# Performance work log

Hardware: AMD Instinct MI355X
Metric: run time of the kernel (lower is better)

Reference implementation:

```python
import jax, jax.numpy as jnp
import numpy as np

EPS_PROJ = 0.004   # float32 branch of _project
EPS_MIN = 1e-15


def _poincare_linear(x, weight_v, weight_g, bias, c):
    c = c.reshape(())
    rc = jnp.sqrt(c)
    # z_unit: column-normalized weight (weight_v / ||weight_v||_col)
    z_unit = weight_v / jnp.maximum(jnp.linalg.norm(weight_v, axis=0), EPS_MIN)  # [in, out]
    # unidirectional Poincare MLR
    drcr = 2.0 * rc * bias                                  # [out]
    rcx = rc * x                                            # [N, in]
    cx2 = jnp.sum(rcx * rcx, axis=-1, keepdims=True)        # [N, 1]
    num = 2.0 * (rcx @ z_unit) * jnp.cosh(drcr) - (1.0 + cx2) * jnp.sinh(drcr)
    mlr = 2.0 * weight_g / rc * jnp.arcsinh(num / jnp.maximum(1.0 - cx2, EPS_MIN))  # [N, out]
    # map back to the ball: sinh, then gyro-half map
    y = jnp.sinh(rc * mlr) / rc
    y = y / (1.0 + jnp.sqrt(1.0 + c * jnp.sum(y * y, axis=-1, keepdims=True)))
    # _project onto ball of curvature k = -c
    k = -c
    maxnorm = (1.0 - EPS_PROJ) / jnp.sqrt(jnp.maximum(jnp.abs(k), EPS_MIN))
    maxnorm = jnp.where(k < 0, maxnorm, jnp.float32(1e15))
    norm = jnp.maximum(jnp.linalg.norm(y, axis=-1, keepdims=True), EPS_MIN)
    return jnp.where(norm > maxnorm, y / norm * maxnorm, y)


def setup_inputs() -> dict:
    key = jax.random.key(0)
    k1, k2, k3 = jax.random.split(key, 3)
    N, IN, OUT = 32768, 1024, 1024
    # points strictly inside the unit Poincare ball (||x|| ~ 0.64)
    x = jax.random.normal(k1, (N, IN), dtype=jnp.float32) * 0.02
    std = (2.0 * IN * OUT) ** (-0.5)
    weight_v = jax.random.normal(k2, (IN, OUT), dtype=jnp.float32) * std
    weight_g = jax.random.uniform(k3, (OUT,), dtype=jnp.float32, minval=0.5, maxval=1.5) * std * (IN ** 0.5)
    bias = jnp.zeros((OUT,), dtype=jnp.float32)
    c = jnp.ones((1,), dtype=jnp.float32)
    return {"x": x, "weight_v": weight_v, "weight_g": weight_g, "bias": bias, "c": c}


def reference(x, weight_v, weight_g, bias, c):
    return _poincare_linear(x, weight_v, weight_g, bias, c)
```

## Files before the change

kernel.cpp:

```cpp
#include <hip/hip_runtime.h>

#define K_DIM 1024
#define N_DIM 1024
#define GRID 256

typedef short v8s __attribute__((ext_vector_type(8)));
typedef float v4f __attribute__((ext_vector_type(4)));

__device__ __forceinline__ unsigned int bf16_rne(float f) {
    unsigned int u = __float_as_uint(f);
    u += 0x7FFFu + ((u >> 16) & 1u);
    return u >> 16;
}

__global__ void prep_w(const float* __restrict__ wv, const float* __restrict__ wg,
                       const float* __restrict__ bias, const float* __restrict__ cptr,
                       float* __restrict__ coshd, float* __restrict__ sinhd,
                       float* __restrict__ gfac, unsigned short* __restrict__ Btf) {
    __shared__ float tile[64 * 65];
    __shared__ float cred[4][64];
    __shared__ float cinv[64];
    const int t = threadIdx.x;
    const int ti = blockIdx.x & 15;
    const int tj = blockIdx.x >> 4;
    {
        const int cj = t & 63, rg = t >> 6;
        const float* wp = wv + (size_t)(rg * 256) * N_DIM + tj * 64 + cj;
        float ss = 0.f;
#pragma unroll 4
        for (int r = 0; r < 256; ++r) {
            float v = wp[(size_t)r * N_DIM];
            ss = fmaf(v, v, ss);
        }
        cred[rg][cj] = ss;
    }
    {
        const int kl = t >> 2, cq = t & 3;
        const float* src = wv + (size_t)(ti * 64 + kl) * N_DIM + tj * 64 + cq * 16;
        float4 fq[4];
#pragma unroll
        for (int i = 0; i < 4; ++i) fq[i] = ((const float4*)src)[i];
        float* dst = &tile[kl * 65 + cq * 16];
#pragma unroll
        for (int i = 0; i < 4; ++i) {
            dst[4 * i + 0] = fq[i].x; dst[4 * i + 1] = fq[i].y;
            dst[4 * i + 2] = fq[i].z; dst[4 * i + 3] = fq[i].w;
        }
    }
    __syncthreads();
    if (t < 64) {
        float s = cred[0][t] + cred[1][t] + cred[2][t] + cred[3][t];
        cinv[t] = 1.0f / fmaxf(sqrtf(s), 1e-15f);
        if (ti == 0) {
            const int col = tj * 64 + t;
            const float rc = sqrtf(cptr[0]);
            float d = 2.0f * rc * bias[col];
            float e = __expf(d), ie = 1.0f / e;
            coshd[col] = 0.5f * (e + ie);
            sinhd[col] = 0.5f * (e - ie);
            gfac[col] = 2.0f * wg[col];
        }
    }
    __syncthreads();
    {
        const int nl = t & 63, kc = t >> 6;
        const float ci = cinv[nl];
        const int nt_g = tj * 4 + (nl >> 4);
#pragma unroll
        for (int h = 0; h < 2; ++h) {
            const int k8g = ti * 8 + kc * 2 + h;
            const int ks_g = k8g >> 2;
            const int L = (nl & 15) | ((k8g & 3) << 4);
            unsigned int p[4];
#pragma unroll
            for (int j = 0; j < 4; ++j) {
                float v0 = tile[(kc * 16 + h * 8 + 2 * j) * 65 + nl] * ci;
                float v1 = tile[(kc * 16 + h * 8 + 2 * j + 1) * 65 + nl] * ci;
                p[j] = bf16_rne(v0) | (bf16_rne(v1) << 16);
            }
            *(uint4*)(Btf + ((size_t)(nt_g * 32 + ks_g) * 64 + L) * 8) =
                make_uint4(p[0], p[1], p[2], p[3]);
        }
    }
}

__device__ __forceinline__ void stage_panel(const float* __restrict__ xp,
                                            unsigned short* __restrict__ Asl,
                                            float* __restrict__ rowssbuf, int t) {
#pragma unroll 2
    for (int it = 0; it < 16; ++it) {
        const int g = it * 512 + t;
        const int row = g >> 7, k8 = g & 127;
        const float4* fp = (const float4*)xp + (size_t)g * 2;
        float4 f0 = fp[0];
        float4 f1 = fp[1];
        float vals[8] = {f0.x, f0.y, f0.z, f0.w, f1.x, f1.y, f1.z, f1.w};
        unsigned int p[4];
        float ss = 0.f;
#pragma unroll
        for (int j = 0; j < 4; ++j) {
            ss = fmaf(vals[2 * j], vals[2 * j], ss);
            ss = fmaf(vals[2 * j + 1], vals[2 * j + 1], ss);
            p[j] = bf16_rne(vals[2 * j]) | (bf16_rne(vals[2 * j + 1]) << 16);
        }
        ss += __shfl_xor(ss, 1);  ss += __shfl_xor(ss, 2);  ss += __shfl_xor(ss, 4);
        ss += __shfl_xor(ss, 8);  ss += __shfl_xor(ss, 16); ss += __shfl_xor(ss, 32);
        if ((t & 63) == 0) atomicAdd(&rowssbuf[row], ss);
        const int mt = row >> 4, lm2 = row & 15, ks = k8 >> 2, qq = k8 & 3;
        const int idx = ((mt * 32 + ks) * 512) + (((lm2 ^ (ks & 7)) | (qq << 4)) * 8);
        *(uint4*)&Asl[idx] = make_uint4(p[0], p[1], p[2], p[3]);
    }
}

__launch_bounds__(512, 2)
__global__ void gemm_fused(const float* __restrict__ x,
                           const unsigned short* __restrict__ Btf,
                           const float* __restrict__ cptr,
                           const float* __restrict__ coshd, const float* __restrict__ sinhd,
                           const float* __restrict__ gfac,
                           float* __restrict__ out, int panels) {
    __shared__ __align__(16) unsigned short As[4 * 32 * 512];
    __shared__ float s_rowss[2][64];
    __shared__ float s_rsum[64];

    const int t = threadIdx.x;
    const int w = t >> 6, L = t & 63;
    const int lm = L & 15, q = L >> 4;
    const int bm = blockIdx.x;

    const float cc = cptr[0];
    const float rc = sqrtf(cc);
    const float two_rc = 2.0f * rc;
    const float halfinvrc = 0.5f / rc;
    const float mn = (cc > 0.f) ? 0.996f / sqrtf(fmaxf(cc, 1e-15f)) : 1e15f;
    float ch[8], sh[8], gf[8];
#pragma unroll
    for (int n = 0; n < 8; ++n) {
        const int col = w * 128 + n * 16 + lm;
        ch[n] = coshd[col]; sh[n] = sinhd[col]; gf[n] = gfac[col];
    }

    const unsigned short* bw = Btf + (size_t)(w * 8) * 32 * 512 + (size_t)L * 8;

    if (t < 64) s_rowss[0][t] = 0.f;
    __syncthreads();
    stage_panel(x + (size_t)bm * 64 * K_DIM, As, s_rowss[0], t);

#pragma unroll 1
    for (int i = 0; i < panels; ++i) {
        const int p = bm + i * GRID;
        const int pb = i & 1, nb = pb ^ 1;
        const bool more = (i + 1 < panels);
        __syncthreads();

        v4f acc[4][8];
#pragma unroll
        for (int a = 0; a < 4; ++a)
#pragma unroll
            for (int b = 0; b < 8; ++b) acc[a][b] = (v4f){0.f, 0.f, 0.f, 0.f};

        v8s bA[8], bB[8];
#pragma unroll
        for (int n = 0; n < 8; ++n)
            bA[n] = *(const v8s*)(bw + (n * 32) * 512);

#pragma unroll 1
        for (int kp = 0; kp < 16; ++kp) {
            const int k0 = kp * 2;
#pragma unroll
            for (int n = 0; n < 8; ++n)
                bB[n] = *(const v8s*)(bw + (n * 32 + k0 + 1) * 512);
            {
                const int lx = ((lm ^ (k0 & 7)) | (q << 4)) * 8;
                v8s a[4];
#pragma unroll
                for (int mt = 0; mt < 4; ++mt)
                    a[mt] = *(const v8s*)&As[(mt * 32 + k0) * 512 + lx];
                __builtin_amdgcn_s_setprio(1);
#pragma unroll
                for (int mt = 0; mt < 4; ++mt)
#pragma unroll
                    for (int n = 0; n < 8; ++n)
                        acc[mt][n] = __builtin_amdgcn_mfma_f32_16x16x32_bf16(
                            a[mt], bA[n], acc[mt][n], 0, 0, 0);
                __builtin_amdgcn_s_setprio(0);
            }
            if (kp < 15) {
#pragma unroll
                for (int n = 0; n < 8; ++n)
                    bA[n] = *(const v8s*)(bw + (n * 32 + k0 + 2) * 512);
            }
            {
                const int lx = ((lm ^ ((k0 + 1) & 7)) | (q << 4)) * 8;
                v8s a[4];
#pragma unroll
                for (int mt = 0; mt < 4; ++mt)
                    a[mt] = *(const v8s*)&As[(mt * 32 + k0 + 1) * 512 + lx];
                __builtin_amdgcn_s_setprio(1);
#pragma unroll
                for (int mt = 0; mt < 4; ++mt)
#pragma unroll
                    for (int n = 0; n < 8; ++n)
                        acc[mt][n] = __builtin_amdgcn_mfma_f32_16x16x32_bf16(
                            a[mt], bB[n], acc[mt][n], 0, 0, 0);
                __builtin_amdgcn_s_setprio(0);
            }
        }

        __syncthreads();
        if (t < 64) { s_rsum[t] = 0.f; if (more) s_rowss[nb][t] = 0.f; }
        __syncthreads();

        if (more) stage_panel(x + (size_t)(p + GRID) * 64 * K_DIM, As, s_rowss[nb], t);

        const float* rb = s_rowss[pb];
#pragma unroll
        for (int mt = 0; mt < 4; ++mt) {
            const int mloc = mt * 16 + q * 4;
            float sx[4];
#pragma unroll
            for (int rr = 0; rr < 4; ++rr) sx[rr] = cc * rb[mloc + rr];
            float rs[4] = {0.f, 0.f, 0.f, 0.f};
#pragma unroll
            for (int n = 0; n < 8; ++n) {
                v4f d = acc[mt][n];
#pragma unroll
                for (int rr = 0; rr < 4; ++rr) {
                    float cx2 = sx[rr];
                    float num = two_rc * d[rr] * ch[n] - (1.0f + cx2) * sh[n];
                    float den = fmaxf(1.0f - cx2, 1e-15f);
                    float tt = num * __builtin_amdgcn_rcpf(den);
                    float as_ = __logf(fabsf(tt) + sqrtf(fmaf(tt, tt, 1.0f)));
                    as_ = copysignf(as_, tt);
                    float u = gf[n] * as_;
                    float e = __expf(u);
                    float y = (e - __builtin_amdgcn_rcpf(e)) * halfinvrc;
                    d[rr] = y;
                    rs[rr] = fmaf(y, y, rs[rr]);
                }
                acc[mt][n] = d;
            }
#pragma unroll
            for (int rr = 0; rr < 4; ++rr) {
                float v = rs[rr];
                v += __shfl_xor(v, 1); v += __shfl_xor(v, 2);
                v += __shfl_xor(v, 4); v += __shfl_xor(v, 8);
                if (lm == 0) atomicAdd(&s_rsum[mloc + rr], v);
            }
        }
        __syncthreads();

#pragma unroll
        for (int mt = 0; mt < 4; ++mt) {
            const int mloc = mt * 16 + q * 4;
            float f[4];
#pragma unroll
            for (int rr = 0; rr < 4; ++rr) {
                const float s = s_rsum[mloc + rr];
                const float scale = 1.0f / (1.0f + sqrtf(fmaf(cc, s, 1.0f)));
                const float nrm = fmaxf(sqrtf(s) * scale, 1e-15f);
                f[rr] = scale * (nrm > mn ? mn / nrm : 1.0f);
            }
#pragma unroll
            for (int rr = 0; rr < 4; ++rr) {
                float* op = out + (size_t)(p * 64 + mloc + rr) * N_DIM + w * 128 + lm;
#pragma unroll
                for (int n = 0; n < 8; ++n) op[n * 16] = acc[mt][n][rr] * f[rr];
            }
        }
    }
}

extern "C" void kernel_launch(void* const* d_in, const int* in_sizes, int n_in,
                              void* d_out, int out_size, void* d_ws, size_t ws_size,
                              hipStream_t stream) {
    const float* x    = (const float*)d_in[0];
    const float* wv   = (const float*)d_in[1];
    const float* wg   = (const float*)d_in[2];
    const float* bias = (const float*)d_in[3];
    const float* cptr = (const float*)d_in[4];
    float* out = (float*)d_out;

    const int OUT = in_sizes[2];
    const int IN  = in_sizes[1] / OUT;
    const int M   = in_sizes[0] / IN;

    float* coshd = (float*)d_ws;
    float* sinhd = coshd + 1024;
    float* gfac  = sinhd + 1024;
    unsigned short* Btf = (unsigned short*)(gfac + 1024);

    prep_w<<<(IN / 64) * (OUT / 64), 256, 0, stream>>>(
        wv, wg, bias, cptr, coshd, sinhd, gfac, Btf);

    const int panels = (M / 64) / GRID;
    gemm_fused<<<GRID, 512, 0, stream>>>(
        x, Btf, cptr, coshd, sinhd, gfac, out, panels);
}
```

Before: 371.0 us.

## Hand-pipeline B global loads with inline asm and explicit vmcnt waits, new LDS swizzle

Rewrites the GEMM inner loop as an explicit two-stage software pipeline. B fragments are loaded with inline global_load_dwordx4 from a scalar base plus per-lane offsets, and waits use explicit s_waitcnt vmcnt(8) with sched barriers so one k-step of loads stays in flight during the MFMAs. The A panel LDS layout gets a new XOR swizzle that also uses the quad index, to cut LDS bank conflicts, and the staging loop unroll goes from 2 to 4. Hand-written waitcnt and asm constrain the compiler's scheduling and depend on exact counts of in-flight loads.

```diff
diff --git a/kernel.cpp b/kernel.cpp
--- a/kernel.cpp
+++ b/kernel.cpp
@@ -6,6 +6,7 @@
 
 typedef short v8s __attribute__((ext_vector_type(8)));
 typedef float v4f __attribute__((ext_vector_type(4)));
+typedef unsigned int v4u __attribute__((ext_vector_type(4)));
 
 __device__ __forceinline__ unsigned int bf16_rne(float f) {
     unsigned int u = __float_as_uint(f);
@@ -87,7 +88,7 @@
 __device__ __forceinline__ void stage_panel(const float* __restrict__ xp,
                                             unsigned short* __restrict__ Asl,
                                             float* __restrict__ rowssbuf, int t) {
-#pragma unroll 2
+#pragma unroll 4
     for (int it = 0; it < 16; ++it) {
         const int g = it * 512 + t;
         const int row = g >> 7, k8 = g & 127;
@@ -106,11 +107,44 @@
         ss += __shfl_xor(ss, 1);  ss += __shfl_xor(ss, 2);  ss += __shfl_xor(ss, 4);
         ss += __shfl_xor(ss, 8);  ss += __shfl_xor(ss, 16); ss += __shfl_xor(ss, 32);
         if ((t & 63) == 0) atomicAdd(&rowssbuf[row], ss);
-        const int mt = row >> 4, lm2 = row & 15, ks = k8 >> 2, qq = k8 & 3;
-        const int idx = ((mt * 32 + ks) * 512) + (((lm2 ^ (ks & 7)) | (qq << 4)) * 8);
+        const int mt = row >> 4, lmr = row & 15, ks = k8 >> 2, qq = k8 & 3;
+        const int S = ((lmr ^ ks ^ (qq << 1)) & 7) | (lmr & 8) | (qq << 4);
+        const int idx = ((mt * 32 + ks) << 9) + (S << 3);
         *(uint4*)&Asl[idx] = make_uint4(p[0], p[1], p[2], p[3]);
     }
 }
+
+__device__ __forceinline__ void bload8(v4u (&buf)[8], const unsigned short* bwu,
+                                       const unsigned* voff, int k) {
+    const char* sb = (const char*)bwu + (size_t)k * 1024;
+#pragma unroll
+    for (int n = 0; n < 8; ++n)
+        asm volatile("global_load_dwordx4 %0, %1, %2"
+                     : "=v"(buf[n]) : "v"(voff[n]), "s"(sb));
+}
+
+__device__ __forceinline__ void aread4(v8s (&ab)[4], const unsigned short* As,
+                                       int cl, int rb, int k) {
+    const int off = (((cl ^ (k & 7)) << 4) | rb);
+#pragma unroll
+    for (int mt = 0; mt < 4; ++mt)
+        ab[mt] = *(const v8s*)((const char*)As + ((mt * 32 + k) << 10) + off);
+}
+
+__device__ __forceinline__ void mmac(v4f (&acc)[4][8], const v8s (&a)[4],
+                                     const v4u (&b)[8]) {
+    __builtin_amdgcn_s_setprio(1);
+#pragma unroll
+    for (int mt = 0; mt < 4; ++mt)
+#pragma unroll
+        for (int n = 0; n < 8; ++n)
+            acc[mt][n] = __builtin_amdgcn_mfma_f32_16x16x32_bf16(
+                a[mt], __builtin_bit_cast(v8s, b[n]), acc[mt][n], 0, 0, 0);
+    __builtin_amdgcn_s_setprio(0);
+}
+
+#define WAITV8 do { asm volatile("s_waitcnt vmcnt(8)"); __builtin_amdgcn_sched_barrier(0); } while (0)
+#define WAITV0 do { asm volatile("s_waitcnt vmcnt(0)"); __builtin_amdgcn_sched_barrier(0); } while (0)
 
 __launch_bounds__(512, 2)
 __global__ void gemm_fused(const float* __restrict__ x,
@@ -128,6 +162,9 @@
     const int lm = L & 15, q = L >> 4;
     const int bm = blockIdx.x;
 
+    const int cl = (lm & 7) ^ ((q << 1) & 7);
+    const int rb = ((lm & 8) << 4) + (q << 8);
+
     const float cc = cptr[0];
     const float rc = sqrtf(cc);
     const float two_rc = 2.0f * rc;
@@ -140,7 +177,11 @@
         ch[n] = coshd[col]; sh[n] = sinhd[col]; gf[n] = gfac[col];
     }
 
-    const unsigned short* bw = Btf + (size_t)(w * 8) * 32 * 512 + (size_t)L * 8;
+    const int wu = __builtin_amdgcn_readfirstlane(w);
+    const unsigned short* bwu = Btf + (size_t)wu * 131072;
+    unsigned voff[8];
+#pragma unroll
+    for (int n = 0; n < 8; ++n) voff[n] = (unsigned)(L * 16 + n * 32768);
 
     if (t < 64) s_rowss[0][t] = 0.f;
     __syncthreads();
@@ -159,53 +200,29 @@
 #pragma unroll
             for (int b = 0; b < 8; ++b) acc[a][b] = (v4f){0.f, 0.f, 0.f, 0.f};
 
-        v8s bA[8], bB[8];
-#pragma unroll
-        for (int n = 0; n < 8; ++n)
-            bA[n] = *(const v8s*)(bw + (n * 32) * 512);
+        v4u b0[8], b1[8];
+        v8s a0[4], a1[4];
+        bload8(b0, bwu, voff, 0);
+        bload8(b1, bwu, voff, 1);
+        aread4(a0, As, cl, rb, 0);
 
 #pragma unroll 1
-        for (int kp = 0; kp < 16; ++kp) {
-            const int k0 = kp * 2;
-#pragma unroll
-            for (int n = 0; n < 8; ++n)
-                bB[n] = *(const v8s*)(bw + (n * 32 + k0 + 1) * 512);
-            {
-                const int lx = ((lm ^ (k0 & 7)) | (q << 4)) * 8;
-                v8s a[4];
-#pragma unroll
-                for (int mt = 0; mt < 4; ++mt)
-                    a[mt] = *(const v8s*)&As[(mt * 32 + k0) * 512 + lx];
-                __builtin_amdgcn_s_setprio(1);
-#pragma unroll
-                for (int mt = 0; mt < 4; ++mt)
-#pragma unroll
-                    for (int n = 0; n < 8; ++n)
-                        acc[mt][n] = __builtin_amdgcn_mfma_f32_16x16x32_bf16(
-                            a[mt], bA[n], acc[mt][n], 0, 0, 0);
-                __builtin_amdgcn_s_setprio(0);
-            }
-            if (kp < 15) {
-#pragma unroll
-                for (int n = 0; n < 8; ++n)
-                    bA[n] = *(const v8s*)(bw + (n * 32 + k0 + 2) * 512);
-            }
-            {
-                const int lx = ((lm ^ ((k0 + 1) & 7)) | (q << 4)) * 8;
-                v8s a[4];
-#pragma unroll
-                for (int mt = 0; mt < 4; ++mt)
-                    a[mt] = *(const v8s*)&As[(mt * 32 + k0 + 1) * 512 + lx];
-                __builtin_amdgcn_s_setprio(1);
-#pragma unroll
-                for (int mt = 0; mt < 4; ++mt)
-#pragma unroll
-                    for (int n = 0; n < 8; ++n)
-                        acc[mt][n] = __builtin_amdgcn_mfma_f32_16x16x32_bf16(
-                            a[mt], bB[n], acc[mt][n], 0, 0, 0);
-                __builtin_amdgcn_s_setprio(0);
-            }
-        }
+        for (int kp = 0; kp < 15; ++kp) {
+            const int k = kp * 2;
+            aread4(a1, As, cl, rb, k + 1);
+            WAITV8;
+            mmac(acc, a0, b0);
+            bload8(b0, bwu, voff, k + 2);
+            aread4(a0, As, cl, rb, k + 2);
+            WAITV8;
+            mmac(acc, a1, b1);
+            bload8(b1, bwu, voff, k + 3);
+        }
+        aread4(a1, As, cl, rb, 31);
+        WAITV8;
+        mmac(acc, a0, b0);
+        WAITV0;
+        mmac(acc, a1, b1);
 
         __syncthreads();
         if (t < 64) { s_rsum[t] = 0.f; if (more) s_rowss[nb][t] = 0.f; }
@@ -213,13 +230,13 @@
 
         if (more) stage_panel(x + (size_t)(p + GRID) * 64 * K_DIM, As, s_rowss[nb], t);
 
-        const float* rb = s_rowss[pb];
+        const float* rbuf = s_rowss[pb];
 #pragma unroll
         for (int mt = 0; mt < 4; ++mt) {
             const int mloc = mt * 16 + q * 4;
             float sx[4];
 #pragma unroll
-            for (int rr = 0; rr < 4; ++rr) sx[rr] = cc * rb[mloc + rr];
+            for (int rr = 0; rr < 4; ++rr) sx[rr] = cc * rbuf[mloc + rr];
             float rs[4] = {0.f, 0.f, 0.f, 0.f};
 #pragma unroll
             for (int n = 0; n < 8; ++n) {
```

New measurement: 359.0 us. -3.2%, faster.

## Replace persistent double-buffered panel loop with one 64-row block per workgroup

Applied to the files above, without the earlier changes.

The persistent 256-block kernel, which double-buffered x panels and overlapped staging of the next panel with the epilogue, is replaced by a grid of M/64 blocks of 1024 threads (16 waves in a 2x8 layout). Each block stages one panel once into a non-swizzled LDS layout, runs a single-buffered MFMA loop, then does the epilogue. The intent is to raise occupancy and let hardware scheduling across blocks hide latency instead of in-kernel software pipelining. The trade-off is losing explicit load/compute overlap, B prefetching, and the LDS swizzle, which may cause bank conflicts. A prep unroll is also raised.

```diff
diff --git a/kernel.cpp b/kernel.cpp
--- a/kernel.cpp
+++ b/kernel.cpp
@@ -2,7 +2,6 @@
 
 #define K_DIM 1024
 #define N_DIM 1024
-#define GRID 256
 
 typedef short v8s __attribute__((ext_vector_type(8)));
 typedef float v4f __attribute__((ext_vector_type(4)));
@@ -27,7 +26,7 @@
         const int cj = t & 63, rg = t >> 6;
         const float* wp = wv + (size_t)(rg * 256) * N_DIM + tj * 64 + cj;
         float ss = 0.f;
-#pragma unroll 4
+#pragma unroll 16
         for (int r = 0; r < 256; ++r) {
             float v = wp[(size_t)r * N_DIM];
             ss = fmaf(v, v, ss);
@@ -84,49 +83,76 @@
     }
 }
 
-__device__ __forceinline__ void stage_panel(const float* __restrict__ xp,
-                                            unsigned short* __restrict__ Asl,
-                                            float* __restrict__ rowssbuf, int t) {
-#pragma unroll 2
-    for (int it = 0; it < 16; ++it) {
-        const int g = it * 512 + t;
-        const int row = g >> 7, k8 = g & 127;
-        const float4* fp = (const float4*)xp + (size_t)g * 2;
-        float4 f0 = fp[0];
-        float4 f1 = fp[1];
-        float vals[8] = {f0.x, f0.y, f0.z, f0.w, f1.x, f1.y, f1.z, f1.w};
-        unsigned int p[4];
-        float ss = 0.f;
-#pragma unroll
-        for (int j = 0; j < 4; ++j) {
-            ss = fmaf(vals[2 * j], vals[2 * j], ss);
-            ss = fmaf(vals[2 * j + 1], vals[2 * j + 1], ss);
-            p[j] = bf16_rne(vals[2 * j]) | (bf16_rne(vals[2 * j + 1]) << 16);
-        }
-        ss += __shfl_xor(ss, 1);  ss += __shfl_xor(ss, 2);  ss += __shfl_xor(ss, 4);
-        ss += __shfl_xor(ss, 8);  ss += __shfl_xor(ss, 16); ss += __shfl_xor(ss, 32);
-        if ((t & 63) == 0) atomicAdd(&rowssbuf[row], ss);
-        const int mt = row >> 4, lm2 = row & 15, ks = k8 >> 2, qq = k8 & 3;
-        const int idx = ((mt * 32 + ks) * 512) + (((lm2 ^ (ks & 7)) | (qq << 4)) * 8);
-        *(uint4*)&Asl[idx] = make_uint4(p[0], p[1], p[2], p[3]);
-    }
-}
-
-__launch_bounds__(512, 2)
+__launch_bounds__(1024, 4)
 __global__ void gemm_fused(const float* __restrict__ x,
                            const unsigned short* __restrict__ Btf,
                            const float* __restrict__ cptr,
                            const float* __restrict__ coshd, const float* __restrict__ sinhd,
                            const float* __restrict__ gfac,
-                           float* __restrict__ out, int panels) {
-    __shared__ __align__(16) unsigned short As[4 * 32 * 512];
-    __shared__ float s_rowss[2][64];
+                           float* __restrict__ out) {
+    __shared__ __align__(16) unsigned short As[4 * 32 * 64 * 8];
+    __shared__ float s_rowss[64];
     __shared__ float s_rsum[64];
 
     const int t = threadIdx.x;
     const int w = t >> 6, L = t & 63;
     const int lm = L & 15, q = L >> 4;
+    const int wm = w >> 3, wn = w & 7;
     const int bm = blockIdx.x;
+    const int r0 = bm * 64;
+
+    if (t < 64) { s_rowss[t] = 0.f; s_rsum[t] = 0.f; }
+    __syncthreads();
+
+#pragma unroll
+    for (int i = 0; i < 8; ++i) {
+        const int flat = w + i * 16;
+        const int mtg = flat >> 5, s = flat & 31;
+        const float* xp = x + (size_t)(r0 + mtg * 16 + lm) * K_DIM + s * 32 + q * 8;
+        float4 f0 = ((const float4*)xp)[0];
+        float4 f1 = ((const float4*)xp)[1];
+        float vals[8] = {f0.x, f0.y, f0.z, f0.w, f1.x, f1.y, f1.z, f1.w};
+        unsigned int p[4];
+        float ss = 0.f;
+#pragma unroll
+        for (int j = 0; j < 4; ++j) {
+            ss = fmaf(vals[2 * j], vals[2 * j], ss);
+            ss = fmaf(vals[2 * j + 1], vals[2 * j + 1], ss);
+            p[j] = bf16_rne(vals[2 * j]) | (bf16_rne(vals[2 * j + 1]) << 16);
+        }
+        *(uint4*)&As[(size_t)(flat * 64 + L) * 8] = make_uint4(p[0], p[1], p[2], p[3]);
+        ss += __shfl_xor(ss, 16); ss += __shfl_xor(ss, 32);
+        if (q == 0) atomicAdd(&s_rowss[mtg * 16 + lm], ss);
+    }
+    __syncthreads();
+
+    v4f acc[2][8];
+#pragma unroll
+    for (int a = 0; a < 2; ++a)
+#pragma unroll
+        for (int b = 0; b < 8; ++b) acc[a][b] = (v4f){0.f, 0.f, 0.f, 0.f};
+
+    const unsigned short* bbase = Btf + (size_t)(wn * 8) * 16384 + (size_t)L * 8;
+    const unsigned short* abase0 = As + (size_t)(wm * 2) * 16384 + (size_t)L * 8;
+    const unsigned short* abase1 = abase0 + 16384;
+
+#pragma unroll 1
+    for (int s = 0; s < 32; ++s) {
+        v8s b[8];
+#pragma unroll
+        for (int j = 0; j < 8; ++j)
+            b[j] = *(const v8s*)(bbase + (size_t)j * 16384 + s * 512);
+        v8s a0 = *(const v8s*)(abase0 + s * 512);
+        v8s a1 = *(const v8s*)(abase1 + s * 512);
+        __builtin_amdgcn_s_setprio(1);
+#pragma unroll
+        for (int n = 0; n < 8; ++n)
+            acc[0][n] = __builtin_amdgcn_mfma_f32_16x16x32_bf16(a0, b[n], acc[0][n], 0, 0, 0);
+#pragma unroll
+        for (int n = 0; n < 8; ++n)
+            acc[1][n] = __builtin_amdgcn_mfma_f32_16x16x32_bf16(a1, b[n], acc[1][n], 0, 0, 0);
+        __builtin_amdgcn_s_setprio(0);
+    }
 
     const float cc = cptr[0];
     const float rc = sqrtf(cc);
@@ -136,137 +162,62 @@
     float ch[8], sh[8], gf[8];
 #pragma unroll
     for (int n = 0; n < 8; ++n) {
-        const int col = w * 128 + n * 16 + lm;
+        const int col = wn * 128 + n * 16 + lm;
         ch[n] = coshd[col]; sh[n] = sinhd[col]; gf[n] = gfac[col];
     }
 
-    const unsigned short* bw = Btf + (size_t)(w * 8) * 32 * 512 + (size_t)L * 8;
-
-    if (t < 64) s_rowss[0][t] = 0.f;
-    __syncthreads();
-    stage_panel(x + (size_t)bm * 64 * K_DIM, As, s_rowss[0], t);
-
-#pragma unroll 1
-    for (int i = 0; i < panels; ++i) {
-        const int p = bm + i * GRID;
-        const int pb = i & 1, nb = pb ^ 1;
-        const bool more = (i + 1 < panels);
-        __syncthreads();
-
-        v4f acc[4][8];
-#pragma unroll
-        for (int a = 0; a < 4; ++a)
-#pragma unroll
-            for (int b = 0; b < 8; ++b) acc[a][b] = (v4f){0.f, 0.f, 0.f, 0.f};
-
-        v8s bA[8], bB[8];
-#pragma unroll
-        for (int n = 0; n < 8; ++n)
-            bA[n] = *(const v8s*)(bw + (n * 32) * 512);
-
-#pragma unroll 1
-        for (int kp = 0; kp < 16; ++kp) {
-            const int k0 = kp * 2;
-#pragma unroll
-            for (int n = 0; n < 8; ++n)
-                bB[n] = *(const v8s*)(bw + (n * 32 + k0 + 1) * 512);
-            {
-                const int lx = ((lm ^ (k0 & 7)) | (q << 4)) * 8;
-                v8s a[4];
-#pragma unroll
-                for (int mt = 0; mt < 4; ++mt)
-                    a[mt] = *(const v8s*)&As[(mt * 32 + k0) * 512 + lx];
-                __builtin_amdgcn_s_setprio(1);
-#pragma unroll
-                for (int mt = 0; mt < 4; ++mt)
-#pragma unroll
-                    for (int n = 0; n < 8; ++n)
-                        acc[mt][n] = __builtin_amdgcn_mfma_f32_16x16x32_bf16(
-                            a[mt], bA[n], acc[mt][n], 0, 0, 0);
-                __builtin_amdgcn_s_setprio(0);
+#pragma unroll
+    for (int mt = 0; mt < 2; ++mt) {
+        const int mloc = wm * 32 + mt * 16 + q * 4;
+        float sx[4];
+#pragma unroll
+        for (int rr = 0; rr < 4; ++rr) sx[rr] = cc * s_rowss[mloc + rr];
+        float rs[4] = {0.f, 0.f, 0.f, 0.f};
+#pragma unroll
+        for (int n = 0; n < 8; ++n) {
+            v4f d = acc[mt][n];
+#pragma unroll
+            for (int rr = 0; rr < 4; ++rr) {
+                float cx2 = sx[rr];
+                float num = two_rc * d[rr] * ch[n] - (1.0f + cx2) * sh[n];
+                float den = fmaxf(1.0f - cx2, 1e-15f);
+                float tt = num * __builtin_amdgcn_rcpf(den);
+                float as_ = __logf(fabsf(tt) + sqrtf(fmaf(tt, tt, 1.0f)));
+                as_ = copysignf(as_, tt);
+                float u = gf[n] * as_;
+                float e = __expf(u);
+                float y = (e - __builtin_amdgcn_rcpf(e)) * halfinvrc;
+                d[rr] = y;
+                rs[rr] = fmaf(y, y, rs[rr]);
             }
-            if (kp < 15) {
-#pragma unroll
-                for (int n = 0; n < 8; ++n)
-                    bA[n] = *(const v8s*)(bw + (n * 32 + k0 + 2) * 512);
-            }
-            {
-                const int lx = ((lm ^ ((k0 + 1) & 7)) | (q << 4)) * 8;
-                v8s a[4];
-#pragma unroll
-                for (int mt = 0; mt < 4; ++mt)
-                    a[mt] = *(const v8s*)&As[(mt * 32 + k0 + 1) * 512 + lx];
-                __builtin_amdgcn_s_setprio(1);
-#pragma unroll
-                for (int mt = 0; mt < 4; ++mt)
-#pragma unroll
-                    for (int n = 0; n < 8; ++n)
-                        acc[mt][n] = __builtin_amdgcn_mfma_f32_16x16x32_bf16(
-                            a[mt], bB[n], acc[mt][n], 0, 0, 0);
-                __builtin_amdgcn_s_setprio(0);
-            }
-        }
-
-        __syncthreads();
-        if (t < 64) { s_rsum[t] = 0.f; if (more) s_rowss[nb][t] = 0.f; }
-        __syncthreads();
-
-        if (more) stage_panel(x + (size_t)(p + GRID) * 64 * K_DIM, As, s_rowss[nb], t);
-
-        const float* rb = s_rowss[pb];
-#pragma unroll
-        for (int mt = 0; mt < 4; ++mt) {
-            const int mloc = mt * 16 + q * 4;
-            float sx[4];
-#pragma unroll
-            for (int rr = 0; rr < 4; ++rr) sx[rr] = cc * rb[mloc + rr];
-            float rs[4] = {0.f, 0.f, 0.f, 0.f};
-#pragma unroll
-            for (int n = 0; n < 8; ++n) {
-                v4f d = acc[mt][n];
-#pragma unroll
-                for (int rr = 0; rr < 4; ++rr) {
-                    float cx2 = sx[rr];
-                    float num = two_rc * d[rr] * ch[n] - (1.0f + cx2) * sh[n];
-                    float den = fmaxf(1.0f - cx2, 1e-15f);
-                    float tt = num * __builtin_amdgcn_rcpf(den);
-                    float as_ = __logf(fabsf(tt) + sqrtf(fmaf(tt, tt, 1.0f)));
-                    as_ = copysignf(as_, tt);
-                    float u = gf[n] * as_;
-                    float e = __expf(u);
-                    float y = (e - __builtin_amdgcn_rcpf(e)) * halfinvrc;
-                    d[rr] = y;
-                    rs[rr] = fmaf(y, y, rs[rr]);
-                }
-                acc[mt][n] = d;
-            }
-#pragma unroll
-            for (int rr = 0; rr < 4; ++rr) {
-                float v = rs[rr];
-                v += __shfl_xor(v, 1); v += __shfl_xor(v, 2);
-                v += __shfl_xor(v, 4); v += __shfl_xor(v, 8);
-                if (lm == 0) atomicAdd(&s_rsum[mloc + rr], v);
-            }
-        }
-        __syncthreads();
-
-#pragma unroll
-        for (int mt = 0; mt < 4; ++mt) {
-            const int mloc = mt * 16 + q * 4;
-            float f[4];
-#pragma unroll
-            for (int rr = 0; rr < 4; ++rr) {
-                const float s = s_rsum[mloc + rr];
-                const float scale = 1.0f / (1.0f + sqrtf(fmaf(cc, s, 1.0f)));
-                const float nrm = fmaxf(sqrtf(s) * scale, 1e-15f);
-                f[rr] = scale * (nrm > mn ? mn / nrm : 1.0f);
-            }
-#pragma unroll
-            for (int rr = 0; rr < 4; ++rr) {
-                float* op = out + (size_t)(p * 64 + mloc + rr) * N_DIM + w * 128 + lm;
-#pragma unroll
-                for (int n = 0; n < 8; ++n) op[n * 16] = acc[mt][n][rr] * f[rr];
-            }
+            acc[mt][n] = d;
+        }
+#pragma unroll
+        for (int rr = 0; rr < 4; ++rr) {
+            float v = rs[rr];
+            v += __shfl_xor(v, 1); v += __shfl_xor(v, 2);
+            v += __shfl_xor(v, 4); v += __shfl_xor(v, 8);
+            if (lm == 0) atomicAdd(&s_rsum[mloc + rr], v);
+        }
+    }
+    __syncthreads();
+
+#pragma unroll
+    for (int mt = 0; mt < 2; ++mt) {
+        const int mloc = wm * 32 + mt * 16 + q * 4;
+        float f[4];
+#pragma unroll
+        for (int rr = 0; rr < 4; ++rr) {
+            const float s = s_rsum[mloc + rr];
+            const float scale = 1.0f / (1.0f + sqrtf(fmaf(cc, s, 1.0f)));
+            const float nrm = fmaxf(sqrtf(s) * scale, 1e-15f);
+            f[rr] = scale * (nrm > mn ? mn / nrm : 1.0f);
+        }
+#pragma unroll
+        for (int rr = 0; rr < 4; ++rr) {
+            float* op = out + (size_t)(r0 + mloc + rr) * N_DIM + wn * 128 + lm;
+#pragma unroll
+            for (int n = 0; n < 8; ++n) op[n * 16] = acc[mt][n][rr] * f[rr];
         }
     }
 }
@@ -293,7 +244,6 @@
     prep_w<<<(IN / 64) * (OUT / 64), 256, 0, stream>>>(
         wv, wg, bias, cptr, coshd, sinhd, gfac, Btf);
 
-    const int panels = (M / 64) / GRID;
-    gemm_fused<<<GRID, 512, 0, stream>>>(
-        x, Btf, cptr, coshd, sinhd, gfac, out, panels);
-}
+    gemm_fused<<<M / 64, 1024, 0, stream>>>(
+        x, Btf, cptr, coshd, sinhd, gfac, out);
+}
```

New measurement: 355.1 us. 4.3% less time.
